# Performance work log

Measured on AMD Instinct MI355X. Metric: run time of the kernel, lower is better.

Reference implementation:

```python
import jax, jax.numpy as jnp
import numpy as np

N_NODES = 100000
N_EDGES = 1200000
D_FEAT = 64
THETA = (1.0, -0.8, 0.4, -0.1)  # polynomial coefficients, k = len(THETA)


def setup_inputs() -> dict:
    key = jax.random.key(0)
    k1, k2, k3 = jax.random.split(key, 3)
    feat = jax.random.normal(k1, (N_NODES, D_FEAT), dtype=jnp.float32)
    src = jax.random.randint(k2, (N_EDGES,), 0, N_NODES, dtype=jnp.int32)
    dst = jax.random.randint(k3, (N_EDGES,), 0, N_NODES, dtype=jnp.int32)
    return {"feat": feat, "src": src, "dst": dst}


def reference(feat, src, dst):
    # in-degrees: number of incoming edges per node (clamped to >= 1)
    deg = jax.ops.segment_sum(jnp.ones((N_EDGES,), feat.dtype), dst, num_segments=N_NODES)
    d_invsqrt = jnp.clip(deg, 1.0, None) ** -0.5  # [N]
    d = d_invsqrt[:, None]  # [N, 1]

    h = THETA[0] * feat
    for k in range(1, len(THETA)):
        # unnLaplacian: feat - D^{-1/2} A^T (D^{-1/2} feat)  (copy_u / sum over edges)
        msg = (feat * d)[src]                                   # [E, F] gather
        agg = jax.ops.segment_sum(msg, dst, num_segments=N_NODES)  # [N, F] scatter-add
        feat = feat - agg * d
        h = h + THETA[k] * feat
    return h
```

## Files before the change

### kernel.cpp

```cpp
#include <hip/hip_runtime.h>

#define D_FEAT 64
#define BSHIFT 8
#define MAXB 512
#define CHUNK 4096

typedef float nfloat4 __attribute__((ext_vector_type(4)));

__device__ inline unsigned short f2bf(float f) {
    unsigned u = __float_as_uint(f);
    unsigned r = u + 0x7fffu + ((u >> 16) & 1u);
    return (unsigned short)(r >> 16);
}
__device__ inline float bflo(unsigned w) { return __uint_as_float(w << 16); }
__device__ inline float bfhi(unsigned w) { return __uint_as_float(w & 0xffff0000u); }

__device__ inline void unpack8(uint4 u, float* v) {
    v[0] = bflo(u.x); v[1] = bfhi(u.x);
    v[2] = bflo(u.y); v[3] = bfhi(u.y);
    v[4] = bflo(u.z); v[5] = bfhi(u.z);
    v[6] = bflo(u.w); v[7] = bfhi(u.w);
}
__device__ inline uint4 pack8(const float* v) {
    uint4 u;
    u.x = (unsigned)f2bf(v[0]) | ((unsigned)f2bf(v[1]) << 16);
    u.y = (unsigned)f2bf(v[2]) | ((unsigned)f2bf(v[3]) << 16);
    u.z = (unsigned)f2bf(v[4]) | ((unsigned)f2bf(v[5]) << 16);
    u.w = (unsigned)f2bf(v[6]) | ((unsigned)f2bf(v[7]) << 16);
    return u;
}

__global__ void pre_kernel(const int* __restrict__ dst, int* __restrict__ mat,
                           int nE, int P, int nblk) {
    __shared__ int lh[MAXB];
    int b = blockIdx.x;
    for (int i = threadIdx.x; i < P; i += blockDim.x) lh[i] = 0;
    __syncthreads();
    int s = b * CHUNK;
    int e1 = s + CHUNK; if (e1 > nE) e1 = nE;
    for (int e = s + threadIdx.x; e < e1; e += blockDim.x)
        atomicAdd(&lh[dst[e] >> BSHIFT], 1);
    __syncthreads();
    for (int i = threadIdx.x; i < P; i += blockDim.x)
        mat[i * nblk + b] = lh[i];
}

__global__ void scan1_kernel(const int* __restrict__ in, int* __restrict__ out,
                             int* __restrict__ bsums, int n) {
    __shared__ int tmp[256];
    int tid = threadIdx.x;
    int i = blockIdx.x * 256 + tid;
    int v = (i < n) ? in[i] : 0;
    tmp[tid] = v;
    __syncthreads();
    for (int off = 1; off < 256; off <<= 1) {
        int t2 = 0;
        if (tid >= off) t2 = tmp[tid - off];
        __syncthreads();
        tmp[tid] += t2;
        __syncthreads();
    }
    if (i < n) out[i] = tmp[tid] - v;
    if (tid == 255) bsums[blockIdx.x] = tmp[255];
}

__global__ void scan2_kernel(int* __restrict__ bsums, int nb) {
    __shared__ int tmp[512];
    int tid = threadIdx.x;
    int v = (tid < nb) ? bsums[tid] : 0;
    tmp[tid] = v;
    __syncthreads();
    for (int off = 1; off < 512; off <<= 1) {
        int t2 = 0;
        if (tid >= off) t2 = tmp[tid - off];
        __syncthreads();
        tmp[tid] += t2;
        __syncthreads();
    }
    if (tid < nb) bsums[tid] = tmp[tid] - v;
}

__global__ void scan3add_kernel(int* __restrict__ matS, const int* __restrict__ bsums,
                                int* __restrict__ bucket_ptr, int n, int nblk,
                                int P, int nE) {
    int i = blockIdx.x * 256 + threadIdx.x;
    if (i < n) {
        int v = matS[i] + bsums[blockIdx.x];
        matS[i] = v;
        if (i % nblk == 0) bucket_ptr[i / nblk] = v;
    }
    if (i == 0) bucket_ptr[P] = nE;
}

__global__ void scatter_part_kernel(const int* __restrict__ src, const int* __restrict__ dst,
                                    const int* __restrict__ matS, unsigned* __restrict__ part,
                                    int nE, int P, int nblk) {
    __shared__ int cur[MAXB];
    for (int i = threadIdx.x; i < P; i += blockDim.x)
        cur[i] = matS[i * nblk + blockIdx.x];
    __syncthreads();
    int s = blockIdx.x * CHUNK;
    int e1 = s + CHUNK; if (e1 > nE) e1 = nE;
    for (int e = s + threadIdx.x; e < e1; e += blockDim.x) {
        int t = dst[e];
        int pos = atomicAdd(&cur[t >> BSHIFT], 1);
        part[pos] = ((unsigned)src[e] << 8) | (unsigned)(t & 255);
    }
}

__global__ void bucket_csr_kernel(const unsigned* __restrict__ part,
                                  const int* __restrict__ bucket_ptr,
                                  int* __restrict__ row_ptr, int* __restrict__ row_end,
                                  float* __restrict__ dv, int* __restrict__ esrc, int nN) {
    __shared__ int hist[256];
    __shared__ int cur[256];
    __shared__ int scanT[256];
    int b = blockIdx.x;
    int tid = threadIdx.x;
    int bp0 = bucket_ptr[b], bp1 = bucket_ptr[b + 1];
    hist[tid] = 0;
    __syncthreads();
    for (int e = bp0 + tid; e < bp1; e += 256)
        atomicAdd(&hist[part[e] & 255u], 1);
    __syncthreads();
    int v = hist[tid];
    scanT[tid] = v;
    __syncthreads();
    for (int off = 1; off < 256; off <<= 1) {
        int t2 = 0;
        if (tid >= off) t2 = scanT[tid - off];
        __syncthreads();
        scanT[tid] += t2;
        __syncthreads();
    }
    int startv = scanT[tid] - v;
    cur[tid] = startv;
    int node = (b << BSHIFT) + tid;
    if (node < nN) {
        float fc = (float)(v < 1 ? 1 : v);
        dv[node] = rsqrtf(fc);
        row_ptr[node] = bp0 + startv;
        row_end[node] = bp0 + startv + v;
    }
    __syncthreads();
    for (int e = bp0 + tid; e < bp1; e += 256) {
        unsigned p = part[e];
        int rank = atomicAdd(&cur[p & 255u], 1);
        esrc[bp0 + rank] = (int)(p >> 8);
    }
}

__global__ void cast_kernel(const float4* __restrict__ f, const float* __restrict__ dv,
                            uint4* __restrict__ g0, uint4* __restrict__ g1,
                            int nN, int n8) {
    int i = blockIdx.x * 256 + threadIdx.x;
    if (i < n8) {
        int node = i >> 3;
        float dt = dv[node];
        float4 a = f[(size_t)i * 2];
        float4 c = f[(size_t)i * 2 + 1];
        float v[8] = {a.x * dt, a.y * dt, a.z * dt, a.w * dt,
                      c.x * dt, c.y * dt, c.z * dt, c.w * dt};
        g0[i] = pack8(v);
    }
    if (blockIdx.x == 0 && threadIdx.x < 8) {
        uint4 z; z.x = z.y = z.z = z.w = 0u;
        g0[(size_t)n8 + threadIdx.x] = z;
        g1[(size_t)n8 + threadIdx.x] = z;
    }
}

__global__ void poly_kernel(const uint4* __restrict__ g_in, uint4* __restrict__ g_out,
                            const int* __restrict__ row_ptr, const int* __restrict__ row_end,
                            const int* __restrict__ esrc, const float* __restrict__ dv,
                            const uint4* __restrict__ g0a, const uint4* __restrict__ g1a,
                            float* __restrict__ h, uint4* __restrict__ zfix,
                            int final_step, int nN) {
    if (zfix && blockIdx.x == 0 && threadIdx.x < 8) {
        uint4 z; z.x = z.y = z.z = z.w = 0u;
        zfix[(size_t)nN * 8 + threadIdx.x] = z;
    }
    int wave = (blockIdx.x * blockDim.x + threadIdx.x) >> 6;
    int lane = threadIdx.x & 63;
    int sub  = lane >> 3;
    int q    = lane & 7;
    int t    = wave * 8 + sub;
    bool valid = (t < nN);
    if (!valid) t = nN - 1;

    int r0 = row_ptr[t], r1 = row_end[t];
    if (!valid) r1 = r0;

    float acc[8];
#pragma unroll
    for (int c = 0; c < 8; ++c) acc[c] = 0.0f;

    int sq = nN;
    { int jc = r0 + q; if (jc < r1) sq = esrc[jc]; }
    int j0 = r0;
    while (j0 < r1) {
        int jn = j0 + 8;
        int sq_n = nN;
        { int jc = jn + q; if (jc < r1) sq_n = esrc[jc]; }
        int m = r1 - j0;
#pragma unroll
        for (int u = 0; u < 4; ++u) {
            int sb = __shfl(sq, (sub << 3) + u, 64);
            uint4 fv = g_in[(size_t)sb * 8 + q];
            float v[8];
            unpack8(fv, v);
#pragma unroll
            for (int c = 0; c < 8; ++c) acc[c] += v[c];
        }
        if (m > 4) {
#pragma unroll
            for (int u = 4; u < 8; ++u) {
                int sb = __shfl(sq, (sub << 3) + u, 64);
                uint4 fv = g_in[(size_t)sb * 8 + q];
                float v[8];
                unpack8(fv, v);
#pragma unroll
                for (int c = 0; c < 8; ++c) acc[c] += v[c];
            }
        }
        sq = sq_n; j0 = jn;
    }

    if (!valid) return;
    size_t idx = (size_t)t * 8 + q;
    float dt = dv[t];
    float d2 = dt * dt;
    float go[8];
    unpack8(g_in[idx], go);
    float gn[8];
#pragma unroll
    for (int c = 0; c < 8; ++c) gn[c] = go[c] - acc[c] * d2;

    if (!final_step) {
        g_out[idx] = pack8(gn);
    } else {
        float g1v[8];
        unpack8(g1a[idx], g1v);
        float g0v[8];
        unpack8(g0a[idx], g0v);
        float di = 1.0f / dt;
        float hv[8];
#pragma unroll
        for (int c = 0; c < 8; ++c)
            hv[c] = (g0v[c] - 0.8f * g1v[c] + 0.4f * go[c] - 0.1f * gn[c]) * di;
        nfloat4 h0 = {hv[0], hv[1], hv[2], hv[3]};
        nfloat4 h1 = {hv[4], hv[5], hv[6], hv[7]};
        nfloat4* hp = (nfloat4*)(h + (size_t)t * 64 + q * 8);
        __builtin_nontemporal_store(h0, hp);
        __builtin_nontemporal_store(h1, hp + 1);
    }
}

extern "C" void kernel_launch(void* const* d_in, const int* in_sizes, int n_in,
                              void* d_out, int out_size, void* d_ws, size_t ws_size,
                              hipStream_t stream) {
    const float* feat = (const float*)d_in[0];
    const int*   src  = (const int*)d_in[1];
    const int*   dst  = (const int*)d_in[2];
    float*       h    = (float*)d_out;

    const int nN = in_sizes[0] / D_FEAT;
    const int nE = in_sizes[1];

    const int P    = (nN + 255) >> 8;
    const int nblk = (nE + CHUNK - 1) / CHUNK;
    const int n    = P * nblk;
    const int nb   = (n + 255) / 256;

    auto align = [](size_t x) { return (x + 255) & ~(size_t)255; };
    char* ws = (char*)d_ws;
    size_t off = 0;
    int*      mat        = (int*)(ws + off);      off += align((size_t)n * 4);
    int*      matS       = (int*)(ws + off);      off += align((size_t)n * 4);
    int*      bsums      = (int*)(ws + off);      off += align(512 * 4);
    int*      bucket_ptr = (int*)(ws + off);      off += align((size_t)(P + 1) * 4);
    int*      row_ptr    = (int*)(ws + off);      off += align((size_t)nN * 4);
    int*      row_end    = (int*)(ws + off);      off += align((size_t)nN * 4);
    float*    dv         = (float*)(ws + off);    off += align((size_t)nN * 4);
    unsigned* part       = (unsigned*)(ws + off); off += align((size_t)nE * 4);
    int*      esrc       = (int*)(ws + off);      off += align((size_t)nE * 4);
    size_t fbBytes = (size_t)(nN + 1) * D_FEAT * 2;
    uint4*    fb0        = (uint4*)(ws + off);    off += align(fbBytes);
    uint4*    fb1        = (uint4*)(ws + off);    off += align(fbBytes);
    uint4*    fb2;
    if (ws_size >= off + fbBytes) {
        fb2 = (uint4*)(ws + off);
    } else {
        fb2 = (uint4*)d_in[0];
    }

    const int n8 = nN * 8;
    const int tb = (n8 + 255) / 256;
    pre_kernel         <<<nblk, 256, 0, stream>>>(dst, mat, nE, P, nblk);
    scan1_kernel       <<<nb, 256, 0, stream>>>(mat, matS, bsums, n);
    scan2_kernel       <<<1, 512, 0, stream>>>(bsums, nb);
    scan3add_kernel    <<<nb, 256, 0, stream>>>(matS, bsums, bucket_ptr, n, nblk, P, nE);
    scatter_part_kernel<<<nblk, 256, 0, stream>>>(src, dst, matS, part, nE, P, nblk);
    bucket_csr_kernel  <<<P, 256, 0, stream>>>(part, bucket_ptr, row_ptr, row_end,
                                               dv, esrc, nN);
    cast_kernel        <<<tb, 256, 0, stream>>>((const float4*)feat, dv, fb0, fb1, nN, n8);

    long long waves = ((long long)nN + 7) / 8;
    int polyBlocks = (int)((waves * 64 + 255) / 256);
    poly_kernel<<<polyBlocks, 256, 0, stream>>>(fb0, fb1, row_ptr, row_end, esrc, dv,
                                                nullptr, nullptr, nullptr, fb2, 0, nN);
    poly_kernel<<<polyBlocks, 256, 0, stream>>>(fb1, fb2, row_ptr, row_end, esrc, dv,
                                                nullptr, nullptr, nullptr, nullptr, 0, nN);
    poly_kernel<<<polyBlocks, 256, 0, stream>>>(fb2, nullptr, row_ptr, row_end, esrc, dv,
                                                fb0, fb1, h, nullptr, 1, nN);
}
```

Before: 195.3 us.

## Split each row's edges into source-range quarters and gather in block-synchronized phases

The CSR build now sorts each destination row's edges into four sub-ranges keyed on bits of the source index, storing four row starts per node. Each wave handles four node groups, and the poly kernel walks all groups through one source quarter at a time, with a __syncthreads between phases. The aim is to keep the gather footprint of a block within a quarter of the feature table at a time, for better cache locality. The cost is more registers (4x8 accumulators), block barriers, fewer blocks, and larger row-pointer storage.

```diff
diff --git a/kernel.cpp b/kernel.cpp
--- a/kernel.cpp
+++ b/kernel.cpp
@@ -4,6 +4,7 @@
 #define BSHIFT 8
 #define MAXB 512
 #define CHUNK 4096
+#define NG 4
 
 typedef float nfloat4 __attribute__((ext_vector_type(4)));
 
@@ -110,20 +111,26 @@
 
 __global__ void bucket_csr_kernel(const unsigned* __restrict__ part,
                                   const int* __restrict__ bucket_ptr,
-                                  int* __restrict__ row_ptr, int* __restrict__ row_end,
+                                  int4* __restrict__ rp4, int* __restrict__ row_end,
                                   float* __restrict__ dv, int* __restrict__ esrc, int nN) {
-    __shared__ int hist[256];
-    __shared__ int cur[256];
+    __shared__ int hist[1024];
+    __shared__ int cur[1024];
     __shared__ int scanT[256];
     int b = blockIdx.x;
     int tid = threadIdx.x;
     int bp0 = bucket_ptr[b], bp1 = bucket_ptr[b + 1];
-    hist[tid] = 0;
-    __syncthreads();
-    for (int e = bp0 + tid; e < bp1; e += 256)
-        atomicAdd(&hist[part[e] & 255u], 1);
-    __syncthreads();
-    int v = hist[tid];
+#pragma unroll
+    for (int i = 0; i < 4; ++i) hist[tid * 4 + i] = 0;
+    __syncthreads();
+    for (int e = bp0 + tid; e < bp1; e += 256) {
+        unsigned p = part[e];
+        int key = (int)(((p & 255u) << 2) | ((p >> 23) & 3u));
+        atomicAdd(&hist[key], 1);
+    }
+    __syncthreads();
+    int h0 = hist[tid * 4], h1 = hist[tid * 4 + 1];
+    int h2 = hist[tid * 4 + 2], h3 = hist[tid * 4 + 3];
+    int v = h0 + h1 + h2 + h3;
     scanT[tid] = v;
     __syncthreads();
     for (int off = 1; off < 256; off <<= 1) {
@@ -134,19 +141,23 @@
         __syncthreads();
     }
     int startv = scanT[tid] - v;
-    cur[tid] = startv;
+    int s0 = bp0 + startv, s1 = s0 + h0, s2 = s1 + h1, s3 = s2 + h2;
+    cur[tid * 4] = s0; cur[tid * 4 + 1] = s1;
+    cur[tid * 4 + 2] = s2; cur[tid * 4 + 3] = s3;
     int node = (b << BSHIFT) + tid;
     if (node < nN) {
         float fc = (float)(v < 1 ? 1 : v);
         dv[node] = rsqrtf(fc);
-        row_ptr[node] = bp0 + startv;
-        row_end[node] = bp0 + startv + v;
+        int4 rp; rp.x = s0; rp.y = s1; rp.z = s2; rp.w = s3;
+        rp4[node] = rp;
+        row_end[node] = s0 + v;
     }
     __syncthreads();
     for (int e = bp0 + tid; e < bp1; e += 256) {
         unsigned p = part[e];
-        int rank = atomicAdd(&cur[p & 255u], 1);
-        esrc[bp0 + rank] = (int)(p >> 8);
+        int key = (int)(((p & 255u) << 2) | ((p >> 23) & 3u));
+        int pos = atomicAdd(&cur[key], 1);
+        esrc[pos] = (int)(p >> 8);
     }
 }
 
@@ -170,89 +181,109 @@
     }
 }
 
-__global__ void poly_kernel(const uint4* __restrict__ g_in, uint4* __restrict__ g_out,
-                            const int* __restrict__ row_ptr, const int* __restrict__ row_end,
-                            const int* __restrict__ esrc, const float* __restrict__ dv,
-                            const uint4* __restrict__ g0a, const uint4* __restrict__ g1a,
-                            float* __restrict__ h, uint4* __restrict__ zfix,
-                            int final_step, int nN) {
+__global__ __launch_bounds__(256, 4)
+void poly_kernel(const uint4* __restrict__ g_in, uint4* __restrict__ g_out,
+                 const int4* __restrict__ rp4, const int* __restrict__ row_end,
+                 const int* __restrict__ esrc, const float* __restrict__ dv,
+                 const uint4* __restrict__ g0a, const uint4* __restrict__ g1a,
+                 float* __restrict__ h, uint4* __restrict__ zfix,
+                 int final_step, int nN) {
     if (zfix && blockIdx.x == 0 && threadIdx.x < 8) {
         uint4 z; z.x = z.y = z.z = z.w = 0u;
         zfix[(size_t)nN * 8 + threadIdx.x] = z;
     }
-    int wave = (blockIdx.x * blockDim.x + threadIdx.x) >> 6;
+    int wave = (blockIdx.x * 256 + (int)threadIdx.x) >> 6;
     int lane = threadIdx.x & 63;
     int sub  = lane >> 3;
     int q    = lane & 7;
-    int t    = wave * 8 + sub;
-    bool valid = (t < nN);
-    if (!valid) t = nN - 1;
-
-    int r0 = row_ptr[t], r1 = row_end[t];
-    if (!valid) r1 = r0;
-
-    float acc[8];
-#pragma unroll
-    for (int c = 0; c < 8; ++c) acc[c] = 0.0f;
-
-    int sq = nN;
-    { int jc = r0 + q; if (jc < r1) sq = esrc[jc]; }
-    int j0 = r0;
-    while (j0 < r1) {
-        int jn = j0 + 8;
-        int sq_n = nN;
-        { int jc = jn + q; if (jc < r1) sq_n = esrc[jc]; }
-        int m = r1 - j0;
-#pragma unroll
-        for (int u = 0; u < 4; ++u) {
-            int sb = __shfl(sq, (sub << 3) + u, 64);
-            uint4 fv = g_in[(size_t)sb * 8 + q];
-            float v[8];
-            unpack8(fv, v);
-#pragma unroll
-            for (int c = 0; c < 8; ++c) acc[c] += v[c];
-        }
-        if (m > 4) {
-#pragma unroll
-            for (int u = 4; u < 8; ++u) {
-                int sb = __shfl(sq, (sub << 3) + u, 64);
-                uint4 fv = g_in[(size_t)sb * 8 + q];
-                float v[8];
-                unpack8(fv, v);
-#pragma unroll
-                for (int c = 0; c < 8; ++c) acc[c] += v[c];
+
+    int4 rp[NG];
+    int  re[NG];
+    float acc[NG][8];
+#pragma unroll
+    for (int k = 0; k < NG; ++k) {
+        int t = (wave * NG + k) * 8 + sub;
+        bool va = (t < nN);
+        int tc = va ? t : (nN - 1);
+        int4 r4 = rp4[tc];
+        int  ren = row_end[tc];
+        if (!va) { r4.x = r4.y = r4.z = r4.w = 0; ren = 0; }
+        rp[k] = r4; re[k] = ren;
+#pragma unroll
+        for (int c = 0; c < 8; ++c) acc[k][c] = 0.0f;
+    }
+
+#pragma unroll
+    for (int r = 0; r < 4; ++r) {
+        if (r) __syncthreads();
+#pragma unroll
+        for (int k = 0; k < NG; ++k) {
+            int s = (r == 0) ? rp[k].x : (r == 1) ? rp[k].y : (r == 2) ? rp[k].z : rp[k].w;
+            int e = (r == 0) ? rp[k].y : (r == 1) ? rp[k].z : (r == 2) ? rp[k].w : re[k];
+            int sq = nN;
+            { int jc = s + q; if (jc < e) sq = esrc[jc]; }
+            int j0 = s;
+            while (j0 < e) {
+                int jn = j0 + 8;
+                int sq_n = nN;
+                { int jc = jn + q; if (jc < e) sq_n = esrc[jc]; }
+                int m = e - j0;
+#pragma unroll
+                for (int u = 0; u < 4; ++u) {
+                    int sb = __shfl(sq, (sub << 3) + u, 64);
+                    uint4 fv = g_in[(size_t)sb * 8 + q];
+                    float v[8];
+                    unpack8(fv, v);
+#pragma unroll
+                    for (int c = 0; c < 8; ++c) acc[k][c] += v[c];
+                }
+                if (m > 4) {
+#pragma unroll
+                    for (int u = 4; u < 8; ++u) {
+                        int sb = __shfl(sq, (sub << 3) + u, 64);
+                        uint4 fv = g_in[(size_t)sb * 8 + q];
+                        float v[8];
+                        unpack8(fv, v);
+#pragma unroll
+                        for (int c = 0; c < 8; ++c) acc[k][c] += v[c];
+                    }
+                }
+                sq = sq_n; j0 = jn;
             }
         }
-        sq = sq_n; j0 = jn;
-    }
-
-    if (!valid) return;
-    size_t idx = (size_t)t * 8 + q;
-    float dt = dv[t];
-    float d2 = dt * dt;
-    float go[8];
-    unpack8(g_in[idx], go);
-    float gn[8];
-#pragma unroll
-    for (int c = 0; c < 8; ++c) gn[c] = go[c] - acc[c] * d2;
-
-    if (!final_step) {
-        g_out[idx] = pack8(gn);
-    } else {
-        float g1v[8];
-        unpack8(g1a[idx], g1v);
-        float g0v[8];
-        unpack8(g0a[idx], g0v);
-        float di = 1.0f / dt;
-        float hv[8];
-#pragma unroll
-        for (int c = 0; c < 8; ++c)
-            hv[c] = (g0v[c] - 0.8f * g1v[c] + 0.4f * go[c] - 0.1f * gn[c]) * di;
-        nfloat4 h0 = {hv[0], hv[1], hv[2], hv[3]};
-        nfloat4 h1 = {hv[4], hv[5], hv[6], hv[7]};
-        nfloat4* hp = (nfloat4*)(h + (size_t)t * 64 + q * 8);
-        __builtin_nontemporal_store(h0, hp);
-        __builtin_nontemporal_store(h1, hp + 1);
+    }
+
+#pragma unroll
+    for (int k = 0; k < NG; ++k) {
+        int t = (wave * NG + k) * 8 + sub;
+        if (t >= nN) continue;
+        size_t idx = (size_t)t * 8 + q;
+        float dt = dv[t];
+        float d2 = dt * dt;
+        float go[8];
+        unpack8(g_in[idx], go);
+        float gn[8];
+#pragma unroll
+        for (int c = 0; c < 8; ++c) gn[c] = go[c] - acc[k][c] * d2;
+
+        if (!final_step) {
+            g_out[idx] = pack8(gn);
+        } else {
+            float g1v[8];
+            unpack8(g1a[idx], g1v);
+            float g0v[8];
+            unpack8(g0a[idx], g0v);
+            float di = 1.0f / dt;
+            float hv[8];
+#pragma unroll
+            for (int c = 0; c < 8; ++c)
+                hv[c] = (g0v[c] - 0.8f * g1v[c] + 0.4f * go[c] - 0.1f * gn[c]) * di;
+            nfloat4 h0 = {hv[0], hv[1], hv[2], hv[3]};
+            nfloat4 h1 = {hv[4], hv[5], hv[6], hv[7]};
+            nfloat4* hp = (nfloat4*)(h + (size_t)t * 64 + q * 8);
+            __builtin_nontemporal_store(h0, hp);
+            __builtin_nontemporal_store(h1, hp + 1);
+        }
     }
 }
 
@@ -279,7 +310,7 @@
     int*      matS       = (int*)(ws + off);      off += align((size_t)n * 4);
     int*      bsums      = (int*)(ws + off);      off += align(512 * 4);
     int*      bucket_ptr = (int*)(ws + off);      off += align((size_t)(P + 1) * 4);
-    int*      row_ptr    = (int*)(ws + off);      off += align((size_t)nN * 4);
+    int4*     rp4        = (int4*)(ws + off);     off += align((size_t)nN * 16);
     int*      row_end    = (int*)(ws + off);      off += align((size_t)nN * 4);
     float*    dv         = (float*)(ws + off);    off += align((size_t)nN * 4);
     unsigned* part       = (unsigned*)(ws + off); off += align((size_t)nE * 4);
@@ -301,16 +332,17 @@
     scan2_kernel       <<<1, 512, 0, stream>>>(bsums, nb);
     scan3add_kernel    <<<nb, 256, 0, stream>>>(matS, bsums, bucket_ptr, n, nblk, P, nE);
     scatter_part_kernel<<<nblk, 256, 0, stream>>>(src, dst, matS, part, nE, P, nblk);
-    bucket_csr_kernel  <<<P, 256, 0, stream>>>(part, bucket_ptr, row_ptr, row_end,
+    bucket_csr_kernel  <<<P, 256, 0, stream>>>(part, bucket_ptr, rp4, row_end,
                                                dv, esrc, nN);
     cast_kernel        <<<tb, 256, 0, stream>>>((const float4*)feat, dv, fb0, fb1, nN, n8);
 
-    long long waves = ((long long)nN + 7) / 8;
-    int polyBlocks = (int)((waves * 64 + 255) / 256);
-    poly_kernel<<<polyBlocks, 256, 0, stream>>>(fb0, fb1, row_ptr, row_end, esrc, dv,
+    long long groups = ((long long)nN + 7) / 8;
+    long long wavesNeeded = (groups + NG - 1) / NG;
+    int polyBlocks = (int)((wavesNeeded + 3) / 4);
+    poly_kernel<<<polyBlocks, 256, 0, stream>>>(fb0, fb1, rp4, row_end, esrc, dv,
                                                 nullptr, nullptr, nullptr, fb2, 0, nN);
-    poly_kernel<<<polyBlocks, 256, 0, stream>>>(fb1, fb2, row_ptr, row_end, esrc, dv,
+    poly_kernel<<<polyBlocks, 256, 0, stream>>>(fb1, fb2, rp4, row_end, esrc, dv,
                                                 nullptr, nullptr, nullptr, nullptr, 0, nN);
-    poly_kernel<<<polyBlocks, 256, 0, stream>>>(fb2, nullptr, row_ptr, row_end, esrc, dv,
+    poly_kernel<<<polyBlocks, 256, 0, stream>>>(fb2, nullptr, rp4, row_end, esrc, dv,
                                                 fb0, fb1, h, nullptr, 1, nN);
 }
```

Result: slower. 225.7 us (+15.6%).
